# Optimization experiments

Measured on AMD Instinct MI355X. Metric: run time of the kernel, lower is better.

The kernel has to match this reference:

```python
import jax, jax.numpy as jnp
import numpy as np

N_NODES = 50000
N_EDGES = 4000   # hyperedges
NNZ = 400000
N_GRAPHS = 64
C = 1024
EPS = 1e-5


def _safe_inv(d):
    return jnp.where(d > 0, 1.0 / d, 0.0)


def hypergraph_conv(x, W, b, node_idx, hyperedge_idx):
    # PyG HypergraphConv (no attention, unit hyperedge weights):
    # out = D^{-1} H B^{-1} H^T (x W) + b
    h = x @ W                                              # [N, C]
    ones = jnp.ones(node_idx.shape[0], dtype=x.dtype)
    Dinv = _safe_inv(jax.ops.segment_sum(ones, node_idx, num_segments=N_NODES))
    Binv = _safe_inv(jax.ops.segment_sum(ones, hyperedge_idx, num_segments=N_EDGES))
    # node -> hyperedge
    m = jax.ops.segment_sum(h[node_idx], hyperedge_idx, num_segments=N_EDGES)
    m = m * Binv[:, None]                                  # [E, C]
    # hyperedge -> node
    out = jax.ops.segment_sum(m[hyperedge_idx], node_idx, num_segments=N_NODES)
    return out * Dinv[:, None] + b


def batch_norm(x, gamma, beta):
    mu = jnp.mean(x, axis=0)
    var = jnp.mean(jnp.square(x - mu), axis=0)
    return (x - mu) * jax.lax.rsqrt(var + EPS) * gamma + beta


def setup_inputs() -> dict:
    key = jax.random.key(0)
    ks = jax.random.split(key, 16)
    s = 1.0 / np.sqrt(C)
    inp = {
        "x": jax.random.normal(ks[0], (N_NODES, C), dtype=jnp.float32),
        "node_idx": jax.random.randint(ks[1], (NNZ,), 0, N_NODES, dtype=jnp.int32),
        "hyperedge_idx": jax.random.randint(ks[2], (NNZ,), 0, N_EDGES, dtype=jnp.int32),
        "batch": jnp.sort(jax.random.randint(ks[3], (N_NODES,), 0, N_GRAPHS, dtype=jnp.int32)),
        "W1": jax.random.normal(ks[4], (C, C), dtype=jnp.float32) * s,
        "b1": jnp.zeros((C,), dtype=jnp.float32),
        "W2": jax.random.normal(ks[5], (C, C), dtype=jnp.float32) * s,
        "b2": jnp.zeros((C,), dtype=jnp.float32),
        "W3": jax.random.normal(ks[6], (C, C), dtype=jnp.float32) * s,
        "b3": jnp.zeros((C,), dtype=jnp.float32),
        "g1": jnp.ones((C,), dtype=jnp.float32), "be1": jnp.zeros((C,), dtype=jnp.float32),
        "g2": jnp.ones((C,), dtype=jnp.float32), "be2": jnp.zeros((C,), dtype=jnp.float32),
        "g3": jnp.ones((C,), dtype=jnp.float32), "be3": jnp.zeros((C,), dtype=jnp.float32),
        "Wfc": jax.random.normal(ks[7], (C, 1), dtype=jnp.float32) * s,
        "bfc": jnp.zeros((1,), dtype=jnp.float32),
    }
    return inp


def reference(x, node_idx, hyperedge_idx, batch, W1, b1, W2, b2, W3, b3,
              g1, be1, g2, be2, g3, be3, Wfc, bfc):
    h = x
    for (W, b, g, be) in ((W1, b1, g1, be1), (W2, b2, g2, be2), (W3, b3, g3, be3)):
        h = hypergraph_conv(h, W, b, node_idx, hyperedge_idx)
        h = jax.nn.relu(batch_norm(h, g, be))  # dropout = identity (eval)
    # global_mean_pool over graph ids
    sums = jax.ops.segment_sum(h, batch, num_segments=N_GRAPHS)      # [G, C]
    cnt = jax.ops.segment_sum(jnp.ones((N_NODES,), h.dtype), batch, num_segments=N_GRAPHS)
    pooled = sums / jnp.maximum(cnt, 1.0)[:, None]
    out = (pooled @ Wfc + bfc).squeeze(-1)                            # [G]
    return jax.nn.sigmoid(out)
```

## Files before the change

kernel.cpp:

```cpp
#include <hip/hip_runtime.h>
#include <cstdint>
#include <cstddef>

#define N_NODES  50000
#define N_EDGES  4000
#define E_PAD    4096
#define NNZ_     400000
#define N_GRAPHS 64
#define C_DIM    1024
#define HALF_C   512
#define PB_BLOCKS 2048
#define BN_EPS   1e-5f

typedef float f32x4  __attribute__((ext_vector_type(4)));
typedef short bf16x4 __attribute__((ext_vector_type(4)));
typedef short bf16x8 __attribute__((ext_vector_type(8)));

__device__ __forceinline__ short f2bf(float f) {
  uint32_t u = __builtin_bit_cast(uint32_t, f);
  u += 0x7fffu + ((u >> 16) & 1u);
  return (short)(u >> 16);
}
__device__ __forceinline__ float bf2f(short s) {
  uint32_t u = ((uint32_t)(uint16_t)s) << 16;
  return __builtin_bit_cast(float, u);
}

__global__ void countDeg(const int* __restrict__ ni, const int* __restrict__ ei,
                         int* __restrict__ nd, int* __restrict__ ed) {
  int i = blockIdx.x * 256 + threadIdx.x;
  if (i < NNZ_) {
    atomicAdd(&nd[ni[i]], 1);
    atomicAdd(&ed[ei[i]], 1);
  }
}

__global__ void exscan(const int* __restrict__ deg, int* __restrict__ off, int n) {
  __shared__ int wsum[16];
  __shared__ int carry_s;
  int t = threadIdx.x, lane = t & 63, w = t >> 6;
  if (t == 0) carry_s = 0;
  __syncthreads();
  for (int base = 0; base < n; base += 1024) {
    int v = (base + t < n) ? deg[base + t] : 0;
    int x = v;
    #pragma unroll
    for (int d = 1; d < 64; d <<= 1) { int y = __shfl_up(x, d); if (lane >= d) x += y; }
    if (lane == 63) wsum[w] = x;
    __syncthreads();
    if (t < 16) {
      int y = wsum[t];
      #pragma unroll
      for (int d = 1; d < 16; d <<= 1) { int z = __shfl_up(y, d); if (t >= d) y += z; }
      wsum[t] = y;
    }
    __syncthreads();
    int c = carry_s;
    int incl = x + (w ? wsum[w - 1] : 0);
    if (base + t < n) off[base + t] = c + incl - v;
    int total = wsum[15];
    __syncthreads();
    if (t == 0) carry_s = c + total;
    __syncthreads();
  }
  if (threadIdx.x == 0) off[n] = carry_s;
}

__global__ void fillCSR(const int* __restrict__ ni, const int* __restrict__ ei,
                        const int* __restrict__ noff, const int* __restrict__ eoff,
                        int* __restrict__ ncur, int* __restrict__ ecur,
                        int* __restrict__ node_edge, int* __restrict__ edge_node) {
  int i = blockIdx.x * 256 + threadIdx.x;
  if (i < NNZ_) {
    int n = ni[i], e = ei[i];
    int pe = eoff[e] + atomicAdd(&ecur[e], 1);
    edge_node[pe] = n;
    int pn = noff[n] + atomicAdd(&ncur[n], 1);
    node_edge[pn] = e;
  }
}

__global__ void invdeg(const int* __restrict__ nd, const int* __restrict__ ed,
                       float* __restrict__ Dinv, float* __restrict__ Binv) {
  int i = blockIdx.x * 256 + threadIdx.x;
  if (i < N_NODES) { int d = nd[i]; Dinv[i] = d > 0 ? 1.f / (float)d : 0.f; }
  if (i < N_EDGES) { int d = ed[i]; Binv[i] = d > 0 ? 1.f / (float)d : 0.f; }
}

__global__ void convertWT(const float* __restrict__ Wm, short* __restrict__ WT) {
  __shared__ float tile[64][65];
  int tx = threadIdx.x & 63, ty = threadIdx.x >> 6;
  int kb = blockIdx.x * 64, nb = blockIdx.y * 64;
  #pragma unroll
  for (int j = 0; j < 64; j += 4)
    tile[j + ty][tx] = Wm[(size_t)(kb + j + ty) * C_DIM + nb + tx];
  __syncthreads();
  #pragma unroll
  for (int j = 0; j < 64; j += 4)
    WT[(size_t)(nb + j + ty) * C_DIM + kb + tx] = f2bf(tile[tx][j + ty]);
}

__global__ void convertX(const float* __restrict__ X, short* __restrict__ Hbf) {
  size_t idx = ((size_t)blockIdx.x * 256 + threadIdx.x) * 8;
  int node = (int)(idx >> 10);
  int c = (int)(idx & 1023);
  int half = c >> 9, off = c & 511;
  float v[8];
  *(f32x4*)&v[0] = *(const f32x4*)&X[idx];
  *(f32x4*)&v[4] = *(const f32x4*)&X[idx + 4];
  bf16x8 ov;
  #pragma unroll
  for (int j = 0; j < 8; ++j) ov[j] = f2bf(v[j]);
  *(bf16x8*)&Hbf[((size_t)half * N_NODES + node) * HALF_C + off] = ov;
}

template <int BN>
__global__ __launch_bounds__(64) void phaseA_bn3(
    const short* __restrict__ Hbf, const int* __restrict__ eoff,
    const int* __restrict__ enode, const float* __restrict__ Binv,
    const float* __restrict__ sc, const float* __restrict__ sh,
    short* __restrict__ Mbf, int half) {
  int t = threadIdx.x;
  int e = blockIdx.x;
  int off = t * 8;
  int gc = half * HALF_C + off;
  if (e >= N_EDGES) {
    bf16x8 z = {0, 0, 0, 0, 0, 0, 0, 0};
    *(bf16x8*)&Mbf[(size_t)e * C_DIM + gc] = z;
    return;
  }
  const short* __restrict__ src = Hbf + (size_t)half * N_NODES * HALF_C;
  float scl[8], shf[8];
  if (BN) {
    *(f32x4*)&scl[0] = *(const f32x4*)&sc[gc];
    *(f32x4*)&scl[4] = *(const f32x4*)&sc[gc + 4];
    *(f32x4*)&shf[0] = *(const f32x4*)&sh[gc];
    *(f32x4*)&shf[4] = *(const f32x4*)&sh[gc + 4];
  }
  int beg = eoff[e], end = eoff[e + 1];
  float a0[8] = {0, 0, 0, 0, 0, 0, 0, 0};
  float a1[8] = {0, 0, 0, 0, 0, 0, 0, 0};
  int i = beg;
  for (; i + 3 < end; i += 4) {
    int n0 = enode[i], n1 = enode[i + 1], n2 = enode[i + 2], n3 = enode[i + 3];
    bf16x8 v0 = *(const bf16x8*)&src[(size_t)n0 * HALF_C + off];
    bf16x8 v1 = *(const bf16x8*)&src[(size_t)n1 * HALF_C + off];
    bf16x8 v2 = *(const bf16x8*)&src[(size_t)n2 * HALF_C + off];
    bf16x8 v3 = *(const bf16x8*)&src[(size_t)n3 * HALF_C + off];
    #pragma unroll
    for (int j = 0; j < 8; ++j) {
      float f0 = bf2f(v0[j]), f1 = bf2f(v1[j]);
      float f2 = bf2f(v2[j]), f3 = bf2f(v3[j]);
      if (BN) {
        f0 = fmaxf(f0 * scl[j] + shf[j], 0.f);
        f1 = fmaxf(f1 * scl[j] + shf[j], 0.f);
        f2 = fmaxf(f2 * scl[j] + shf[j], 0.f);
        f3 = fmaxf(f3 * scl[j] + shf[j], 0.f);
      }
      a0[j] += f0 + f2;
      a1[j] += f1 + f3;
    }
  }
  for (; i < end; ++i) {
    bf16x8 v = *(const bf16x8*)&src[(size_t)enode[i] * HALF_C + off];
    #pragma unroll
    for (int j = 0; j < 8; ++j) {
      float f = bf2f(v[j]);
      if (BN) f = fmaxf(f * scl[j] + shf[j], 0.f);
      a0[j] += f;
    }
  }
  float bi = Binv[e];
  bf16x8 ov;
  #pragma unroll
  for (int j = 0; j < 8; ++j) ov[j] = f2bf((a0[j] + a1[j]) * bi);
  *(bf16x8*)&Mbf[(size_t)e * C_DIM + gc] = ov;
}

__global__ __launch_bounds__(256) void gemm_bf16(const short* __restrict__ A,
                                                 const short* __restrict__ BT,
                                                 short* __restrict__ Cc) {
  __shared__ __align__(16) short As[2][128 * 32];
  __shared__ __align__(16) short Bs[2][128 * 32];
  const int tid = threadIdx.x;
  const int w = tid >> 6;
  const int lane = tid & 63;
  const int bm = blockIdx.x, bn = blockIdx.y;
  const int wr = w >> 1, wc = w & 1;
  const int fr = lane & 15, kg = lane >> 4;
  const int qa = w * 2;
  const int srow = lane >> 2;
  const int skof = (lane & 3) * 8;

  f32x4 acc[4][4] = {};

  auto stage = [&](int ks, int buf) {
    #pragma unroll
    for (int c2 = 0; c2 < 2; ++c2) {
      int q = qa + c2;
      int row = q * 16 + srow;
      size_t gA = (size_t)(bm * 128 + row) * C_DIM + ks * 32 + skof;
      size_t gB = (size_t)(bn * 128 + row) * C_DIM + ks * 32 + skof;
      __builtin_amdgcn_global_load_lds(
          (__attribute__((address_space(1))) void*)(A + gA),
          (__attribute__((address_space(3))) void*)(&As[buf][q * 512]), 16, 0, 0);
      __builtin_amdgcn_global_load_lds(
          (__attribute__((address_space(1))) void*)(BT + gB),
          (__attribute__((address_space(3))) void*)(&Bs[buf][q * 512]), 16, 0, 0);
    }
  };
  auto compute = [&](int buf) {
    bf16x8 a[4], b[4];
    #pragma unroll
    for (int m = 0; m < 4; ++m)
      a[m] = *(const bf16x8*)&As[buf][(wr * 64 + m * 16 + fr) * 32 + kg * 8];
    #pragma unroll
    for (int n = 0; n < 4; ++n)
      b[n] = *(const bf16x8*)&Bs[buf][(wc * 64 + n * 16 + fr) * 32 + kg * 8];
    #pragma unroll
    for (int m = 0; m < 4; ++m)
      #pragma unroll
      for (int n = 0; n < 4; ++n)
        acc[m][n] = __builtin_amdgcn_mfma_f32_16x16x32_bf16(a[m], b[n], acc[m][n], 0, 0, 0);
  };

  stage(0, 0);
  __syncthreads();
  for (int ks = 0; ks < 31; ++ks) {
    stage(ks + 1, (ks + 1) & 1);
    compute(ks & 1);
    __syncthreads();
  }
  compute(1);

  const int row0 = bm * 128 + wr * 64 + kg * 4;
  const int col0 = bn * 128 + wc * 64 + fr;
  #pragma unroll
  for (int m = 0; m < 4; ++m) {
    #pragma unroll
    for (int n = 0; n < 4; ++n) {
      int r = row0 + m * 16, cc = col0 + n * 16;
      #pragma unroll
      for (int j = 0; j < 4; ++j)
        Cc[(size_t)(r + j) * C_DIM + cc] = f2bf(acc[m][n][j]);
    }
  }
}

__global__ void phaseB_fused3(const short* __restrict__ M, const int* __restrict__ noff,
                              const int* __restrict__ nedge, const float* __restrict__ Dinv,
                              const float* __restrict__ bias, short* __restrict__ Hp,
                              float* __restrict__ ps, float* __restrict__ pq) {
  int t = threadIdx.x;
  int c = t * 4;
  int half = c >> 9, off = c & 511;
  short* __restrict__ Hdst = Hp + (size_t)half * N_NODES * HALF_C;
  int b = blockIdx.x;
  f32x4 bias4 = *(const f32x4*)&bias[c];
  f32x4 bsum = {0.f, 0.f, 0.f, 0.f}, bsq = {0.f, 0.f, 0.f, 0.f};
  for (int n = b; n < N_NODES; n += PB_BLOCKS) {
    int beg = noff[n], end = noff[n + 1];
    float a0[4] = {0, 0, 0, 0}, a1[4] = {0, 0, 0, 0};
    int i = beg;
    for (; i + 3 < end; i += 4) {
      int e0 = nedge[i], e1 = nedge[i + 1], e2 = nedge[i + 2], e3 = nedge[i + 3];
      bf16x4 v0 = *(const bf16x4*)&M[(size_t)e0 * C_DIM + c];
      bf16x4 v1 = *(const bf16x4*)&M[(size_t)e1 * C_DIM + c];
      bf16x4 v2 = *(const bf16x4*)&M[(size_t)e2 * C_DIM + c];
      bf16x4 v3 = *(const bf16x4*)&M[(size_t)e3 * C_DIM + c];
      #pragma unroll
      for (int j = 0; j < 4; ++j) {
        a0[j] += bf2f(v0[j]) + bf2f(v2[j]);
        a1[j] += bf2f(v1[j]) + bf2f(v3[j]);
      }
    }
    for (; i < end; ++i) {
      bf16x4 v = *(const bf16x4*)&M[(size_t)nedge[i] * C_DIM + c];
      #pragma unroll
      for (int j = 0; j < 4; ++j) a0[j] += bf2f(v[j]);
    }
    float di = Dinv[n];
    bf16x4 ob;
    f32x4 orr;
    #pragma unroll
    for (int j = 0; j < 4; ++j) {
      float o = (a0[j] + a1[j]) * di + bias4[j];
      ob[j] = f2bf(o);
      orr[j] = bf2f(ob[j]);
    }
    *(bf16x4*)&Hdst[(size_t)n * HALF_C + off] = ob;
    bsum += orr;
    bsq += orr * orr;
  }
  *(f32x4*)&ps[(size_t)b * C_DIM + c] = bsum;
  *(f32x4*)&pq[(size_t)b * C_DIM + c] = bsq;
}

__global__ void reduceP(const float* __restrict__ ps, const float* __restrict__ pq,
                        float* __restrict__ ps2, float* __restrict__ pq2) {
  int i = blockIdx.x;
  int c = blockIdx.y * 256 + threadIdx.x;
  float s = 0.f, q = 0.f;
  for (int p = i * 256; p < (i + 1) * 256; ++p) {
    s += ps[(size_t)p * C_DIM + c];
    q += pq[(size_t)p * C_DIM + c];
  }
  ps2[(size_t)i * C_DIM + c] = s;
  pq2[(size_t)i * C_DIM + c] = q;
}

__global__ void bnfinal2(const float* __restrict__ ps2, const float* __restrict__ pq2,
                         const float* __restrict__ g, const float* __restrict__ be,
                         float* __restrict__ scale, float* __restrict__ shift) {
  int c = blockIdx.x * 256 + threadIdx.x;
  float s = 0.f, q = 0.f;
  #pragma unroll
  for (int p = 0; p < 8; ++p) {
    s += ps2[(size_t)p * C_DIM + c];
    q += pq2[(size_t)p * C_DIM + c];
  }
  const float invN = 1.f / (float)N_NODES;
  float mu = s * invN;
  float var = q * invN - mu * mu;
  float rs = rsqrtf(var + BN_EPS);
  float scl = g[c] * rs;
  scale[c] = scl;
  shift[c] = be[c] - mu * scl;
}

__global__ void finaldot_bf(const short* __restrict__ Hp, const float* __restrict__ sc,
                            const float* __restrict__ sh, const float* __restrict__ Wfc,
                            float* __restrict__ rows) {
  int row = blockIdx.x * 4 + (threadIdx.x >> 6);
  int lane = threadIdx.x & 63;
  if (row >= N_NODES) return;
  float s = 0.f;
  #pragma unroll
  for (int j = 0; j < 2; ++j) {
    int c = j * HALF_C + lane * 8;
    bf16x8 v = *(const bf16x8*)&Hp[((size_t)j * N_NODES + row) * HALF_C + lane * 8];
    float a[8], b[8], w[8];
    *(f32x4*)&a[0] = *(const f32x4*)&sc[c];
    *(f32x4*)&a[4] = *(const f32x4*)&sc[c + 4];
    *(f32x4*)&b[0] = *(const f32x4*)&sh[c];
    *(f32x4*)&b[4] = *(const f32x4*)&sh[c + 4];
    *(f32x4*)&w[0] = *(const f32x4*)&Wfc[c];
    *(f32x4*)&w[4] = *(const f32x4*)&Wfc[c + 4];
    #pragma unroll
    for (int k = 0; k < 8; ++k)
      s += fmaxf(bf2f(v[k]) * a[k] + b[k], 0.f) * w[k];
  }
  #pragma unroll
  for (int off = 32; off; off >>= 1) s += __shfl_down(s, off);
  if (lane == 0) rows[row] = s;
}

__global__ void poolbin(const float* __restrict__ rows, const int* __restrict__ batch,
                        float* __restrict__ gsum, int* __restrict__ gcnt) {
  __shared__ float bins[N_GRAPHS];
  __shared__ int cbin[N_GRAPHS];
  int t = threadIdx.x;
  if (t < N_GRAPHS) { bins[t] = 0.f; cbin[t] = 0; }
  __syncthreads();
  int quad = blockIdx.x * 256 + t;
  if (quad * 4 < N_NODES) {
    f32x4 r = *(const f32x4*)&rows[quad * 4];
    int4 bi = *(const int4*)&batch[quad * 4];
    int g0 = bi.x;
    float acc = r[0];
    int cc = 1;
    int gn[3] = {bi.y, bi.z, bi.w};
    float rn[3] = {r[1], r[2], r[3]};
    #pragma unroll
    for (int j = 0; j < 3; ++j) {
      if (gn[j] == g0) { acc += rn[j]; ++cc; }
      else {
        atomicAdd(&bins[g0], acc);
        atomicAdd(&cbin[g0], cc);
        g0 = gn[j]; acc = rn[j]; cc = 1;
      }
    }
    atomicAdd(&bins[g0], acc);
    atomicAdd(&cbin[g0], cc);
  }
  __syncthreads();
  if (t < N_GRAPHS && cbin[t] > 0) {
    atomicAdd(&gsum[t], bins[t]);
    atomicAdd(&gcnt[t], cbin[t]);
  }
}

__global__ void finalout(const float* __restrict__ gsum, const int* __restrict__ gcnt,
                         const float* __restrict__ bfc, float* __restrict__ out) {
  int g = threadIdx.x;
  float cnt = (float)(gcnt[g] > 0 ? gcnt[g] : 1);
  float v = gsum[g] / cnt + bfc[0];
  out[g] = 1.f / (1.f + expf(-v));
}

extern "C" void kernel_launch(void* const* d_in, const int* in_sizes, int n_in,
                              void* d_out, int out_size, void* d_ws, size_t ws_size,
                              hipStream_t stream) {
  const float* x        = (const float*)d_in[0];
  const int*   node_idx = (const int*)d_in[1];
  const int*   hedge_idx= (const int*)d_in[2];
  const int*   batch    = (const int*)d_in[3];
  const float* W[3]  = {(const float*)d_in[4], (const float*)d_in[6], (const float*)d_in[8]};
  const float* bb[3] = {(const float*)d_in[5], (const float*)d_in[7], (const float*)d_in[9]};
  const float* g[3]  = {(const float*)d_in[10], (const float*)d_in[12], (const float*)d_in[14]};
  const float* be[3] = {(const float*)d_in[11], (const float*)d_in[13], (const float*)d_in[15]};
  const float* Wfc   = (const float*)d_in[16];
  const float* bfc   = (const float*)d_in[17];
  float* out = (float*)d_out;

  char* ws = (char*)d_ws;
  size_t o = 0;
  auto take = [&](size_t bytes) -> char* {
    char* p = ws + o;
    o += (bytes + 255) & ~(size_t)255;
    return p;
  };
  short* Xbf  = (short*)take((size_t)N_NODES * C_DIM * 2);
  short* Hp   = (short*)take((size_t)N_NODES * C_DIM * 2);
  short* Mbf  = (short*)take((size_t)E_PAD * C_DIM * 2);
  short* WT   = (short*)take((size_t)C_DIM * C_DIM * 2);
  short* Mw   = (short*)take((size_t)E_PAD * C_DIM * 2);
  char*  zgrp = take(432512);
  int*   node_deg = (int*)zgrp;
  int*   edge_deg = (int*)(zgrp + 200000);
  int*   node_cur = (int*)(zgrp + 216000);
  int*   edge_cur = (int*)(zgrp + 416000);
  float* gsum     = (float*)(zgrp + 432000);
  int*   gcnt     = (int*)(zgrp + 432256);
  int* node_off  = (int*)take((N_NODES + 1) * 4);
  int* edge_off  = (int*)take((N_EDGES + 1) * 4);
  int* node_edge = (int*)take((size_t)NNZ_ * 4);
  int* edge_node = (int*)take((size_t)NNZ_ * 4);
  float* Dinv = (float*)take(N_NODES * 4);
  float* Binv = (float*)take(N_EDGES * 4);
  float* scale = (float*)take(4096);
  float* shift = (float*)take(4096);
  float* part_s = (float*)take((size_t)PB_BLOCKS * C_DIM * 4);
  float* part_q = (float*)take((size_t)PB_BLOCKS * C_DIM * 4);
  float* ps2    = (float*)take((size_t)8 * C_DIM * 4);
  float* pq2    = (float*)take((size_t)8 * C_DIM * 4);
  float* rows   = (float*)take((size_t)N_NODES * 4);

  hipMemsetAsync(zgrp, 0, 432512, stream);

  countDeg<<<(NNZ_ + 255) / 256, 256, 0, stream>>>(node_idx, hedge_idx, node_deg, edge_deg);
  exscan<<<1, 1024, 0, stream>>>(edge_deg, edge_off, N_EDGES);
  exscan<<<1, 1024, 0, stream>>>(node_deg, node_off, N_NODES);
  fillCSR<<<(NNZ_ + 255) / 256, 256, 0, stream>>>(node_idx, hedge_idx, node_off, edge_off,
                                                  node_cur, edge_cur, node_edge, edge_node);
  invdeg<<<(N_NODES + 255) / 256, 256, 0, stream>>>(node_deg, edge_deg, Dinv, Binv);

  const int cgrid = (int)((size_t)N_NODES * C_DIM / (8 * 256));
  convertX<<<cgrid, 256, 0, stream>>>(x, Xbf);
  for (int L = 0; L < 3; ++L) {
    const short* src = (L == 0) ? Xbf : Hp;
    for (int half = 0; half < 2; ++half) {
      if (L == 0)
        phaseA_bn3<0><<<E_PAD, 64, 0, stream>>>(src, edge_off, edge_node, Binv,
                                                nullptr, nullptr, Mbf, half);
      else
        phaseA_bn3<1><<<E_PAD, 64, 0, stream>>>(src, edge_off, edge_node, Binv,
                                                scale, shift, Mbf, half);
    }
    convertWT<<<dim3(16, 16), 256, 0, stream>>>(W[L], WT);
    gemm_bf16<<<dim3(E_PAD / 128, C_DIM / 128), 256, 0, stream>>>(Mbf, WT, Mw);
    phaseB_fused3<<<PB_BLOCKS, 256, 0, stream>>>(Mw, node_off, node_edge, Dinv, bb[L],
                                                 Hp, part_s, part_q);
    reduceP<<<dim3(8, 4), 256, 0, stream>>>(part_s, part_q, ps2, pq2);
    bnfinal2<<<4, 256, 0, stream>>>(ps2, pq2, g[L], be[L], scale, shift);
  }
  finaldot_bf<<<(N_NODES + 3) / 4, 256, 0, stream>>>(Hp, scale, shift, Wfc, rows);
  poolbin<<<(N_NODES / 4 + 255) / 256, 256, 0, stream>>>(rows, batch, gsum, gcnt);
  finalout<<<1, 64, 0, stream>>>(gsum, gcnt, bfc, out);
}
```

Before: 1.114 ms.

## Parallelize degree prefix scans and batch weight conversion and phaseA launches

Replaces the single-block serial exclusive scans over node and edge degrees with a three-stage multi-block scan (per-block sums, a single-wave scan of the block sums, and a final per-block scan). All three weight matrices are converted to transposed bf16 in one launch up front instead of once per layer. The two half-channel phaseA launches per layer are merged into one 2D grid. The intent is to cut serialized launch and single-block latency, at the cost of extra workspace and a few more small scan kernels.

```diff
diff --git a/kernel.cpp b/kernel.cpp
--- a/kernel.cpp
+++ b/kernel.cpp
@@ -35,35 +35,56 @@
   }
 }
 
-__global__ void exscan(const int* __restrict__ deg, int* __restrict__ off, int n) {
-  __shared__ int wsum[16];
-  __shared__ int carry_s;
-  int t = threadIdx.x, lane = t & 63, w = t >> 6;
-  if (t == 0) carry_s = 0;
+__global__ void scan_part(const int* __restrict__ deg, int* __restrict__ bsum, int n) {
+  __shared__ int ws[4];
+  int b = blockIdx.x, t = threadIdx.x;
+  int base = b * 1024 + t * 4;
+  int s = 0;
+  #pragma unroll
+  for (int k = 0; k < 4; ++k) {
+    int i = base + k;
+    if (i < n) s += deg[i];
+  }
+  #pragma unroll
+  for (int d = 32; d; d >>= 1) s += __shfl_down(s, d);
+  int lane = t & 63, w = t >> 6;
+  if (lane == 0) ws[w] = s;
   __syncthreads();
-  for (int base = 0; base < n; base += 1024) {
-    int v = (base + t < n) ? deg[base + t] : 0;
-    int x = v;
-    #pragma unroll
-    for (int d = 1; d < 64; d <<= 1) { int y = __shfl_up(x, d); if (lane >= d) x += y; }
-    if (lane == 63) wsum[w] = x;
-    __syncthreads();
-    if (t < 16) {
-      int y = wsum[t];
-      #pragma unroll
-      for (int d = 1; d < 16; d <<= 1) { int z = __shfl_up(y, d); if (t >= d) y += z; }
-      wsum[t] = y;
-    }
-    __syncthreads();
-    int c = carry_s;
-    int incl = x + (w ? wsum[w - 1] : 0);
-    if (base + t < n) off[base + t] = c + incl - v;
-    int total = wsum[15];
-    __syncthreads();
-    if (t == 0) carry_s = c + total;
-    __syncthreads();
-  }
-  if (threadIdx.x == 0) off[n] = carry_s;
+  if (t == 0) bsum[b] = ws[0] + ws[1] + ws[2] + ws[3];
+}
+
+__global__ void scan_mid(int* __restrict__ bsum, int nb, int* __restrict__ off, int n) {
+  int t = threadIdx.x;
+  int v = (t < nb) ? bsum[t] : 0;
+  int orig = v;
+  #pragma unroll
+  for (int d = 1; d < 64; d <<= 1) { int y = __shfl_up(v, d); if (t >= d) v += y; }
+  if (t < nb) bsum[t] = v - orig;
+  if (t == 63) off[n] = v;
+}
+
+__global__ void scan_final(const int* __restrict__ deg, const int* __restrict__ bsum,
+                           int* __restrict__ off, int n) {
+  __shared__ int ws[4];
+  int b = blockIdx.x, t = threadIdx.x, lane = t & 63, w = t >> 6;
+  int base = b * 1024 + t * 4;
+  int v[4];
+  #pragma unroll
+  for (int k = 0; k < 4; ++k) v[k] = (base + k < n) ? deg[base + k] : 0;
+  int tsum = v[0] + v[1] + v[2] + v[3];
+  int incl = tsum;
+  #pragma unroll
+  for (int d = 1; d < 64; d <<= 1) { int y = __shfl_up(incl, d); if (lane >= d) incl += y; }
+  if (lane == 63) ws[w] = incl;
+  __syncthreads();
+  int woff = 0;
+  for (int j = 0; j < w; ++j) woff += ws[j];
+  int run = bsum[b] + woff + (incl - tsum);
+  #pragma unroll
+  for (int k = 0; k < 4; ++k) {
+    if (base + k < n) off[base + k] = run;
+    run += v[k];
+  }
 }
 
 __global__ void fillCSR(const int* __restrict__ ni, const int* __restrict__ ei,
@@ -87,8 +108,11 @@
   if (i < N_EDGES) { int d = ed[i]; Binv[i] = d > 0 ? 1.f / (float)d : 0.f; }
 }
 
-__global__ void convertWT(const float* __restrict__ Wm, short* __restrict__ WT) {
+__global__ void convertWT(const float* __restrict__ W0, const float* __restrict__ W1,
+                          const float* __restrict__ W2, short* __restrict__ WT3) {
   __shared__ float tile[64][65];
+  const float* Wm = (blockIdx.z == 0) ? W0 : (blockIdx.z == 1) ? W1 : W2;
+  short* WT = WT3 + (size_t)blockIdx.z * C_DIM * C_DIM;
   int tx = threadIdx.x & 63, ty = threadIdx.x >> 6;
   int kb = blockIdx.x * 64, nb = blockIdx.y * 64;
   #pragma unroll
@@ -119,9 +143,10 @@
     const short* __restrict__ Hbf, const int* __restrict__ eoff,
     const int* __restrict__ enode, const float* __restrict__ Binv,
     const float* __restrict__ sc, const float* __restrict__ sh,
-    short* __restrict__ Mbf, int half) {
+    short* __restrict__ Mbf) {
   int t = threadIdx.x;
   int e = blockIdx.x;
+  int half = blockIdx.y;
   int off = t * 8;
   int gc = half * HALF_C + off;
   if (e >= N_EDGES) {
@@ -423,7 +448,7 @@
   short* Xbf  = (short*)take((size_t)N_NODES * C_DIM * 2);
   short* Hp   = (short*)take((size_t)N_NODES * C_DIM * 2);
   short* Mbf  = (short*)take((size_t)E_PAD * C_DIM * 2);
-  short* WT   = (short*)take((size_t)C_DIM * C_DIM * 2);
+  short* WT3  = (short*)take((size_t)3 * C_DIM * C_DIM * 2);
   short* Mw   = (short*)take((size_t)E_PAD * C_DIM * 2);
   char*  zgrp = take(432512);
   int*   node_deg = (int*)zgrp;
@@ -436,6 +461,8 @@
   int* edge_off  = (int*)take((N_EDGES + 1) * 4);
   int* node_edge = (int*)take((size_t)NNZ_ * 4);
   int* edge_node = (int*)take((size_t)NNZ_ * 4);
+  int* bsumN = (int*)take(256);
+  int* bsumE = (int*)take(256);
   float* Dinv = (float*)take(N_NODES * 4);
   float* Binv = (float*)take(N_EDGES * 4);
   float* scale = (float*)take(4096);
@@ -448,27 +475,32 @@
 
   hipMemsetAsync(zgrp, 0, 432512, stream);
 
+  const int nbN = (N_NODES + 1023) / 1024;
+  const int nbE = (N_EDGES + 1023) / 1024;
   countDeg<<<(NNZ_ + 255) / 256, 256, 0, stream>>>(node_idx, hedge_idx, node_deg, edge_deg);
-  exscan<<<1, 1024, 0, stream>>>(edge_deg, edge_off, N_EDGES);
-  exscan<<<1, 1024, 0, stream>>>(node_deg, node_off, N_NODES);
+  scan_part<<<nbE, 256, 0, stream>>>(edge_deg, bsumE, N_EDGES);
+  scan_mid<<<1, 64, 0, stream>>>(bsumE, nbE, edge_off, N_EDGES);
+  scan_final<<<nbE, 256, 0, stream>>>(edge_deg, bsumE, edge_off, N_EDGES);
+  scan_part<<<nbN, 256, 0, stream>>>(node_deg, bsumN, N_NODES);
+  scan_mid<<<1, 64, 0, stream>>>(bsumN, nbN, node_off, N_NODES);
+  scan_final<<<nbN, 256, 0, stream>>>(node_deg, bsumN, node_off, N_NODES);
   fillCSR<<<(NNZ_ + 255) / 256, 256, 0, stream>>>(node_idx, hedge_idx, node_off, edge_off,
                                                   node_cur, edge_cur, node_edge, edge_node);
   invdeg<<<(N_NODES + 255) / 256, 256, 0, stream>>>(node_deg, edge_deg, Dinv, Binv);
 
   const int cgrid = (int)((size_t)N_NODES * C_DIM / (8 * 256));
   convertX<<<cgrid, 256, 0, stream>>>(x, Xbf);
+  convertWT<<<dim3(16, 16, 3), 256, 0, stream>>>(W[0], W[1], W[2], WT3);
   for (int L = 0; L < 3; ++L) {
     const short* src = (L == 0) ? Xbf : Hp;
-    for (int half = 0; half < 2; ++half) {
-      if (L == 0)
-        phaseA_bn3<0><<<E_PAD, 64, 0, stream>>>(src, edge_off, edge_node, Binv,
-                                                nullptr, nullptr, Mbf, half);
-      else
-        phaseA_bn3<1><<<E_PAD, 64, 0, stream>>>(src, edge_off, edge_node, Binv,
-                                                scale, shift, Mbf, half);
-    }
-    convertWT<<<dim3(16, 16), 256, 0, stream>>>(W[L], WT);
-    gemm_bf16<<<dim3(E_PAD / 128, C_DIM / 128), 256, 0, stream>>>(Mbf, WT, Mw);
+    if (L == 0)
+      phaseA_bn3<0><<<dim3(E_PAD, 2), 64, 0, stream>>>(src, edge_off, edge_node, Binv,
+                                                       nullptr, nullptr, Mbf);
+    else
+      phaseA_bn3<1><<<dim3(E_PAD, 2), 64, 0, stream>>>(src, edge_off, edge_node, Binv,
+                                                       scale, shift, Mbf);
+    gemm_bf16<<<dim3(E_PAD / 128, C_DIM / 128), 256, 0, stream>>>(
+        Mbf, WT3 + (size_t)L * C_DIM * C_DIM, Mw);
     phaseB_fused3<<<PB_BLOCKS, 256, 0, stream>>>(Mw, node_off, node_edge, Dinv, bb[L],
                                                  Hp, part_s, part_q);
     reduceP<<<dim3(8, 4), 256, 0, stream>>>(part_s, part_q, ps2, pq2);
```

New measurement: 1.071 ms. 3.8% less time.
